# Optimization experiments

Measured on AMD Instinct MI355X. Metric: run time of the kernel, lower is better.

## Reference

```python
import jax, jax.numpy as jnp
import numpy as np

H = 1024      # hidden_size
I = 2048      # intermediate_size
E = 32        # num_routed_experts
B, S = 4, 2048


def setup_inputs() -> dict:
    key = jax.random.key(0)
    ks = jax.random.split(key, 8)
    scale = 0.02
    inp = {
        "hidden_states": jax.random.normal(ks[0], (B, S, H), dtype=jnp.float32),
        # router gate: stored [H, E] so logits = x @ gate_w
        "gate_w": jax.random.normal(ks[1], (H, E), dtype=jnp.float32) * scale,
        # shared SwiGLU (num_shared_experts=1), weights stored [in, out]
        "shared_gate_w": jax.random.normal(ks[2], (H, I), dtype=jnp.float32) * scale,
        "shared_up_w": jax.random.normal(ks[3], (H, I), dtype=jnp.float32) * scale,
        "shared_down_w": jax.random.normal(ks[4], (I, H), dtype=jnp.float32) * scale,
        # routed grouped SwiGLU, weights stored [E, in, out] (matches GroupedLinear)
        "routed_gate_w": jax.random.normal(ks[5], (E, H, I), dtype=jnp.float32) * scale,
        "routed_up_w": jax.random.normal(ks[6], (E, H, I), dtype=jnp.float32) * scale,
        "routed_down_w": jax.random.normal(ks[7], (E, I, H), dtype=jnp.float32) * scale,
    }
    return inp


def _grouped_mm(a, w, group_sizes):
    # a: [T, in], w: [E, in, out], group_sizes: [E] int32 -> [T, out]
    return jax.lax.ragged_dot(a, w, group_sizes)


def _swiglu(x, gw, uw, dw):
    return (jax.nn.silu(x @ gw) * (x @ uw)) @ dw


def reference(hidden_states, gate_w, shared_gate_w, shared_up_w, shared_down_w,
              routed_gate_w, routed_up_w, routed_down_w):
    b, s, h = hidden_states.shape
    x = hidden_states.reshape(-1, h)                      # [T, H]

    # ---- shared expert ----
    shared_out = _swiglu(x, shared_gate_w, shared_up_w, shared_down_w)

    # ---- router: top-1 ----
    logits = x @ gate_w                                   # [T, E]
    topk_ids = jnp.argmax(logits, axis=-1)                # [T]
    topk_val = jnp.max(logits, axis=-1)                   # [T]
    scores = jax.nn.sigmoid(topk_val)[:, None]            # [T, 1]
    xs = x * scores                                       # scale tokens by router score

    # ---- dispatch: sort tokens by expert id ----
    tokens_per_expert = jnp.zeros((E,), jnp.int32).at[topk_ids].add(1)
    order = jnp.argsort(topk_ids)                         # token ids sorted by expert
    sorted_x = xs[order]                                  # [T, H]

    # ---- grouped SwiGLU experts ----
    g = _grouped_mm(sorted_x, routed_gate_w, tokens_per_expert)   # [T, I]
    u = _grouped_mm(sorted_x, routed_up_w, tokens_per_expert)     # [T, I]
    d = _grouped_mm(jax.nn.silu(g) * u, routed_down_w, tokens_per_expert)  # [T, H]

    # ---- combine: unsort back to token order ----
    inv = jnp.argsort(order)
    routed_out = d[inv]

    return (shared_out + routed_out).reshape(b, s, h)
```

## Files before the change

### kernel.cpp

```cpp
#include <hip/hip_runtime.h>
#include <stdint.h>
#include <stddef.h>

#define TOK 8192
#define H 1024
#define IDIM 2048
#define NE 32
#define BM 128
#define BN 64
#define BK 64
#define MAX_TILES 96

typedef __attribute__((ext_vector_type(8))) short short8;
typedef __attribute__((ext_vector_type(4))) float f32x4;
typedef __attribute__((ext_vector_type(4))) float float4v;
typedef __attribute__((ext_vector_type(2))) unsigned int uint2v;
typedef __attribute__((ext_vector_type(4))) unsigned int uint4v;


__device__ __forceinline__ unsigned short f2bf(float x) {
  unsigned u = __builtin_bit_cast(unsigned, x);
  u += 0x7fffu + ((u >> 16) & 1u);
  return (unsigned short)(u >> 16);
}

__device__ __forceinline__ float bf2f(unsigned short h) {
  unsigned u = ((unsigned)h) << 16;
  return __builtin_bit_cast(float, u);
}

__device__ __forceinline__ unsigned cvtpk(float lo, float hi) {
  unsigned r;
  asm("v_cvt_pk_bf16_f32 %0, %1, %2" : "=v"(r) : "v"(lo), "v"(hi));
  return r;
}

__device__ __forceinline__ void gll16(const void* g, void* l) {
  __builtin_amdgcn_global_load_lds(
      (const __attribute__((address_space(1))) unsigned int*)g,
      (__attribute__((address_space(3))) unsigned int*)l, 16, 0, 0);
}

__device__ __forceinline__ f32x4 mfma16(short8 a, short8 b, f32x4 c) {
  return __builtin_amdgcn_mfma_f32_16x16x32_bf16(a, b, c, 0, 0, 0);
}

__device__ __forceinline__ int wswz(int n) {
  return ((n ^ (n >> 2)) & 7) << 4;
}


__global__ __launch_bounds__(256) void router_kernel(
    const float* __restrict__ x, const float* __restrict__ gw,
    unsigned short* __restrict__ xbf, unsigned short* __restrict__ xsbf,
    int* __restrict__ expert_id, int* __restrict__ counts)
{
  __shared__ float xl[8 * H];
  __shared__ float plog[8][8][NE];
  __shared__ float sscore[8];
  const int tid = threadIdx.x;
  const long t0 = (long)blockIdx.x * 8;

  const float4v* src = (const float4v*)(x + t0 * H);
  float4v* dst = (float4v*)xl;
  #pragma unroll
  for (int i = 0; i < 8; ++i) dst[tid + i * 256] = src[tid + i * 256];
  __syncthreads();

  {
    const int e = tid & 31, c = tid >> 5;
    float acc[8] = {0, 0, 0, 0, 0, 0, 0, 0};
    const float* gp = gw + (c * 128) * NE + e;
    for (int h = 0; h < 128; ++h) {
      float g = gp[h * NE];
      const float* xr = xl + (c * 128 + h);
      #pragma unroll
      for (int tk = 0; tk < 8; ++tk) acc[tk] += xr[tk * H] * g;
    }
    #pragma unroll
    for (int tk = 0; tk < 8; ++tk) plog[c][tk][e] = acc[tk];
  }
  __syncthreads();
  {
    const int e = tid & 31, tok = tid >> 5;
    float lg = 0.f;
    #pragma unroll
    for (int c = 0; c < 8; ++c) lg += plog[c][tok][e];
    float m = lg; int be = e;
    #pragma unroll
    for (int mask = 16; mask >= 1; mask >>= 1) {
      float om = __shfl_xor(m, mask);
      int   oe = __shfl_xor(be, mask);
      if (om > m || (om == m && oe < be)) { m = om; be = oe; }
    }
    if (e == 0) {
      sscore[tok] = 1.f / (1.f + __expf(-m));
      expert_id[t0 + tok] = be;
      atomicAdd(&counts[be], 1);
    }
  }
  __syncthreads();
  {
    const float sc = sscore[tid >> 5];
    const int base = (tid >> 5) * H + (tid & 31) * 32;
    #pragma unroll
    for (int i = 0; i < 4; ++i) {
      uint4v vx, vs;
      #pragma unroll
      for (int q = 0; q < 4; ++q) {
        const float a = xl[base + i * 8 + 2 * q];
        const float b = xl[base + i * 8 + 2 * q + 1];
        vx[q] = cvtpk(a, b);
        vs[q] = cvtpk(a * sc, b * sc);
      }
      *(uint4v*)(xbf  + t0 * H + base + i * 8) = vx;
      *(uint4v*)(xsbf + t0 * H + base + i * 8) = vs;
    }
  }
}


__global__ void scan_kernel(const int* __restrict__ counts, int* __restrict__ offsets,
                            int* __restrict__ cursor, int* __restrict__ tile_e,
                            int* __restrict__ tile_p, int* __restrict__ n_tiles)
{
  if (threadIdx.x != 0) return;
  int off = 0, nt = 0;
  for (int e = 0; e < NE; ++e) {
    offsets[e] = off; cursor[e] = off;
    int cc = counts[e];
    for (int k = 0; k < cc; k += BM) { tile_e[nt] = e; tile_p[nt] = off + k; ++nt; }
    off += cc;
  }
  offsets[NE] = off;
  n_tiles[0] = nt;
}


__global__ __launch_bounds__(256) void perm_kernel(
    const int* __restrict__ expert_id, int* __restrict__ cursor, int* __restrict__ perm)
{
  int t = blockIdx.x * 256 + threadIdx.x;
  int e = expert_id[t];
  int pos = atomicAdd(&cursor[e], 1);
  perm[pos] = t;
}


template<bool ROUTED, bool APERM, int KD, int ND, int EPI>
__global__ __launch_bounds__(256, 4) void gemm_kernel(
    const unsigned short* __restrict__ A,
    const float* __restrict__ Wall,
    float* __restrict__ outf,
    unsigned short* __restrict__ outh,
    const int* __restrict__ perm, const int* __restrict__ tile_e,
    const int* __restrict__ tile_p, const int* __restrict__ offsets,
    const int* __restrict__ n_tiles)
{
  __shared__ short Alds[2][BM * BK];
  __shared__ short Wlds[BN * BK];

  const int tid = threadIdx.x;
  const int wave = tid >> 6, lane = tid & 63;

  int row0, row_end;
  const float* W;
  if constexpr (ROUTED) {
    if ((int)blockIdx.x >= *n_tiles) return;
    const int e = tile_e[blockIdx.x];
    row0 = tile_p[blockIdx.x];
    row_end = offsets[e + 1];
    W = Wall + (size_t)e * KD * ND;
  } else {
    row0 = blockIdx.x * BM; row_end = row0 + BM;
    W = Wall;
  }
  const int n0 = blockIdx.y * BN;

  const unsigned short* asrc[4];
  int aoff[4];
  #pragma unroll
  for (int i = 0; i < 4; ++i) {
    const int r = wave * 32 + i * 8 + (lane >> 3);
    int p = row0 + r;
    if (ROUTED && p >= row_end) p = row0;
    int grow = p;
    if constexpr (ROUTED && APERM) grow = perm[p];
    const int cb = ((lane & 7) * 16) ^ ((r & 7) << 4);
    asrc[i] = A + (size_t)grow * KD + (cb >> 1);
    aoff[i] = (wave * 32 + i * 8) * BK;
  }

  const int wq = tid >> 4;
  const int wc = tid & 15;

  f32x4 acc[2][4] = {};
  float4v w4[4];

  auto stageA = [&](int kt) {
    short* base = Alds[kt & 1];
    #pragma unroll
    for (int i = 0; i < 4; ++i) gll16(asrc[i] + kt * BK, base + aoff[i]);
  };
  auto loadW = [&](int kt) {
    const int k0 = kt * BK;
    #pragma unroll
    for (int r = 0; r < 4; ++r)
      w4[r] = *(const float4v*)(W + (size_t)(k0 + wq * 4 + r) * ND + (n0 + wc * 4));
  };
  auto writeW = [&]() {
    #pragma unroll
    for (int j = 0; j < 4; ++j) {
      const int n = wc * 4 + j;
      const int cb = (wq * 8) ^ wswz(n);
      uint2v pw;
      pw.x = cvtpk(w4[0][j], w4[1][j]);
      pw.y = cvtpk(w4[2][j], w4[3][j]);
      *(uint2v*)((char*)Wlds + n * 128 + cb) = pw;
    }
  };
  auto compute = [&](int kt) {
    const char* ab = (const char*)Alds[kt & 1];
    #pragma unroll
    for (int kk = 0; kk < 2; ++kk) {
      short8 af[2];
      #pragma unroll
      for (int m = 0; m < 2; ++m) {
        const int r = wave * 32 + m * 16 + (lane & 15);
        const int cb = (kk * 64 + ((lane >> 4) * 16)) ^ ((r & 7) << 4);
        af[m] = *(const short8*)(ab + r * 128 + cb);
      }
      #pragma unroll
      for (int nf = 0; nf < 4; ++nf) {
        const int n = nf * 16 + (lane & 15);
        const int cb = (kk * 64 + ((lane >> 4) * 16)) ^ wswz(n);
        short8 bw = *(const short8*)((const char*)Wlds + n * 128 + cb);
        #pragma unroll
        for (int m = 0; m < 2; ++m) acc[m][nf] = mfma16(af[m], bw, acc[m][nf]);
      }
    }
  };

  stageA(0);
  loadW(0);
  writeW();
  __syncthreads();

  #pragma unroll 1
  for (int kt = 0; kt < KD / BK - 1; ++kt) {
    stageA(kt + 1);
    loadW(kt + 1);
    compute(kt);
    __syncthreads();
    writeW();
    __syncthreads();
  }
  compute(KD / BK - 1);

  #pragma unroll
  for (int m = 0; m < 2; ++m)
    #pragma unroll
    for (int nf = 0; nf < 4; ++nf) {
      const int col = n0 + nf * 16 + (lane & 15);
      #pragma unroll
      for (int j = 0; j < 4; ++j) {
        const int row = row0 + wave * 32 + m * 16 + ((lane >> 4) * 4) + j;
        if (ROUTED && row >= row_end) continue;
        const float v = acc[m][nf][j];
        if constexpr (EPI == 0) {
          outh[(size_t)row * ND + col] = f2bf(v);
        } else if constexpr (EPI == 1) {
          const float u = bf2f(outh[(size_t)row * ND + col]);
          const float s = v / (1.f + __expf(-v));
          outh[(size_t)row * ND + col] = f2bf(s * u);
        } else if constexpr (EPI == 2) {
          outf[(size_t)row * ND + col] = v;
        } else {
          const int t = perm[row];
          outf[(size_t)t * ND + col] += v;
        }
      }
    }
}


extern "C" void kernel_launch(void* const* d_in, const int* in_sizes, int n_in,
                              void* d_out, int out_size, void* d_ws, size_t ws_size,
                              hipStream_t stream) {
  (void)in_sizes; (void)n_in; (void)out_size; (void)ws_size;
  const float* x      = (const float*)d_in[0];
  const float* gate_w = (const float*)d_in[1];
  const float* sgw    = (const float*)d_in[2];
  const float* suw    = (const float*)d_in[3];
  const float* sdw    = (const float*)d_in[4];
  const float* rgw    = (const float*)d_in[5];
  const float* ruw    = (const float*)d_in[6];
  const float* rdw    = (const float*)d_in[7];
  float* out = (float*)d_out;

  char* ws = (char*)d_ws;
  unsigned short* xbf  = (unsigned short*)(ws + 0);
  unsigned short* xsbf = (unsigned short*)(ws + 16777216);
  unsigned short* act  = (unsigned short*)(ws + 33554432);
  int* perm      = (int*)(ws + 67108864);
  int* expert_id = (int*)(ws + 67141632);
  int* counts    = (int*)(ws + 67174400);
  int* offsets   = (int*)(ws + 67174528);
  int* cursor    = (int*)(ws + 67174784);
  int* tile_e    = (int*)(ws + 67174912);
  int* tile_p    = (int*)(ws + 67175424);
  int* n_tiles   = (int*)(ws + 67175936);

  hipMemsetAsync(counts, 0, NE * sizeof(int), stream);
  router_kernel<<<TOK / 8, 256, 0, stream>>>(x, gate_w, xbf, xsbf, expert_id, counts);
  scan_kernel<<<1, 64, 0, stream>>>(counts, offsets, cursor, tile_e, tile_p, n_tiles);
  perm_kernel<<<TOK / 256, 256, 0, stream>>>(expert_id, cursor, perm);

  gemm_kernel<false, false, H, IDIM, 0><<<dim3(TOK / BM, IDIM / BN), 256, 0, stream>>>(
      xbf, suw, nullptr, act, perm, tile_e, tile_p, offsets, n_tiles);
  gemm_kernel<false, false, H, IDIM, 1><<<dim3(TOK / BM, IDIM / BN), 256, 0, stream>>>(
      xbf, sgw, nullptr, act, perm, tile_e, tile_p, offsets, n_tiles);
  gemm_kernel<false, false, IDIM, H, 2><<<dim3(TOK / BM, H / BN), 256, 0, stream>>>(
      act, sdw, out, nullptr, perm, tile_e, tile_p, offsets, n_tiles);

  gemm_kernel<true, true, H, IDIM, 0><<<dim3(MAX_TILES, IDIM / BN), 256, 0, stream>>>(
      xsbf, ruw, nullptr, act, perm, tile_e, tile_p, offsets, n_tiles);
  gemm_kernel<true, true, H, IDIM, 1><<<dim3(MAX_TILES, IDIM / BN), 256, 0, stream>>>(
      xsbf, rgw, nullptr, act, perm, tile_e, tile_p, offsets, n_tiles);
  gemm_kernel<true, false, IDIM, H, 3><<<dim3(MAX_TILES, H / BN), 256, 0, stream>>>(
      act, rdw, out, nullptr, perm, tile_e, tile_p, offsets, n_tiles);
}
```

Before: 742.6 us.

## Pre-transpose weights to bf16 and use 128x128 tiles with async B loads

Adds a transpose-and-convert kernel that writes every weight matrix (shared and all 32 routed experts) as K-contiguous bf16 into workspace on each call. The GEMM then loads both A and B straight into LDS with global_load_lds, computes a 128x128 tile per block (4x4 MFMA fragments per wave), and applies a grid swizzle for L2 locality. This drops the in-loop fp32 load, convert and LDS write of weights, but adds a full read of all fp32 weights plus a bf16 write each call (about 800MB of traffic even for experts that receive no tokens), and it removes the double-buffered A pipeline.

```diff
diff --git a/kernel.cpp b/kernel.cpp
--- a/kernel.cpp
+++ b/kernel.cpp
@@ -7,14 +7,12 @@
 #define IDIM 2048
 #define NE 32
 #define BM 128
-#define BN 64
 #define BK 64
 #define MAX_TILES 96
 
 typedef __attribute__((ext_vector_type(8))) short short8;
 typedef __attribute__((ext_vector_type(4))) float f32x4;
 typedef __attribute__((ext_vector_type(4))) float float4v;
-typedef __attribute__((ext_vector_type(2))) unsigned int uint2v;
 typedef __attribute__((ext_vector_type(4))) unsigned int uint4v;
 
 
@@ -45,8 +43,43 @@
   return __builtin_amdgcn_mfma_f32_16x16x32_bf16(a, b, c, 0, 0, 0);
 }
 
-__device__ __forceinline__ int wswz(int n) {
-  return ((n ^ (n >> 2)) & 7) << 4;
+
+__global__ __launch_bounds__(256) void tconv_kernel(
+    const float* __restrict__ src0, unsigned short* __restrict__ dst0,
+    int K, int N)
+{
+  __shared__ float t[64][65];
+  const size_t mat = (size_t)K * N;
+  const float* src = src0 + (size_t)blockIdx.z * mat;
+  unsigned short* dst = dst0 + (size_t)blockIdx.z * mat;
+  const int k0 = blockIdx.x * 64, n0 = blockIdx.y * 64;
+  const int tid = threadIdx.x;
+  {
+    const int r = tid >> 4;
+    const int c = (tid & 15) * 4;
+    #pragma unroll
+    for (int i = 0; i < 4; ++i) {
+      float4v v = *(const float4v*)(src + (size_t)(k0 + r + i * 16) * N + (n0 + c));
+      t[r + i * 16][c + 0] = v[0];
+      t[r + i * 16][c + 1] = v[1];
+      t[r + i * 16][c + 2] = v[2];
+      t[r + i * 16][c + 3] = v[3];
+    }
+  }
+  __syncthreads();
+  {
+    const int n = tid >> 2;
+    const int kc = (tid & 3) * 16;
+    uint4v o0, o1;
+    #pragma unroll
+    for (int q = 0; q < 4; ++q) {
+      o0[q] = cvtpk(t[kc + 2 * q][n],     t[kc + 2 * q + 1][n]);
+      o1[q] = cvtpk(t[kc + 8 + 2 * q][n], t[kc + 8 + 2 * q + 1][n]);
+    }
+    unsigned short* dp = dst + (size_t)(n0 + n) * K + (k0 + kc);
+    *(uint4v*)dp = o0;
+    *(uint4v*)(dp + 8) = o1;
+  }
 }
 
 
@@ -148,123 +181,96 @@
 
 
 template<bool ROUTED, bool APERM, int KD, int ND, int EPI>
-__global__ __launch_bounds__(256, 4) void gemm_kernel(
+__global__ __launch_bounds__(256, 4) void bgemm_kernel(
     const unsigned short* __restrict__ A,
-    const float* __restrict__ Wall,
+    const unsigned short* __restrict__ BT,
     float* __restrict__ outf,
     unsigned short* __restrict__ outh,
     const int* __restrict__ perm, const int* __restrict__ tile_e,
     const int* __restrict__ tile_p, const int* __restrict__ offsets,
     const int* __restrict__ n_tiles)
 {
-  __shared__ short Alds[2][BM * BK];
-  __shared__ short Wlds[BN * BK];
+  __shared__ short Al[BM * BK];
+  __shared__ short Bl[128 * BK];
 
   const int tid = threadIdx.x;
   const int wave = tid >> 6, lane = tid & 63;
+  const int wm = wave >> 1, wn = wave & 1;
+
+  const int nx = gridDim.x;
+  const int nwg = nx * gridDim.y;
+  const int flat = blockIdx.y * nx + blockIdx.x;
+  const int swz = (flat & 7) * (nwg >> 3) + (flat >> 3);
+  const int bx = swz % nx, by = swz / nx;
 
   int row0, row_end;
-  const float* W;
+  const unsigned short* Bt;
   if constexpr (ROUTED) {
-    if ((int)blockIdx.x >= *n_tiles) return;
-    const int e = tile_e[blockIdx.x];
-    row0 = tile_p[blockIdx.x];
+    if (bx >= *n_tiles) return;
+    const int e = tile_e[bx];
+    row0 = tile_p[bx];
     row_end = offsets[e + 1];
-    W = Wall + (size_t)e * KD * ND;
+    Bt = BT + (size_t)e * KD * ND;
   } else {
-    row0 = blockIdx.x * BM; row_end = row0 + BM;
-    W = Wall;
-  }
-  const int n0 = blockIdx.y * BN;
-
-  const unsigned short* asrc[4];
-  int aoff[4];
+    row0 = bx * BM; row_end = row0 + BM;
+    Bt = BT;
+  }
+  const int n0 = by * 128;
+
+  const unsigned short *asrc[4], *bsrc[4];
+  int soff[4];
   #pragma unroll
   for (int i = 0; i < 4; ++i) {
     const int r = wave * 32 + i * 8 + (lane >> 3);
     int p = row0 + r;
     if (ROUTED && p >= row_end) p = row0;
-    int grow = p;
-    if constexpr (ROUTED && APERM) grow = perm[p];
+    int arow = p;
+    if constexpr (ROUTED && APERM) arow = perm[p];
     const int cb = ((lane & 7) * 16) ^ ((r & 7) << 4);
-    asrc[i] = A + (size_t)grow * KD + (cb >> 1);
-    aoff[i] = (wave * 32 + i * 8) * BK;
-  }
-
-  const int wq = tid >> 4;
-  const int wc = tid & 15;
-
-  f32x4 acc[2][4] = {};
-  float4v w4[4];
-
-  auto stageA = [&](int kt) {
-    short* base = Alds[kt & 1];
-    #pragma unroll
-    for (int i = 0; i < 4; ++i) gll16(asrc[i] + kt * BK, base + aoff[i]);
-  };
-  auto loadW = [&](int kt) {
-    const int k0 = kt * BK;
-    #pragma unroll
-    for (int r = 0; r < 4; ++r)
-      w4[r] = *(const float4v*)(W + (size_t)(k0 + wq * 4 + r) * ND + (n0 + wc * 4));
-  };
-  auto writeW = [&]() {
-    #pragma unroll
-    for (int j = 0; j < 4; ++j) {
-      const int n = wc * 4 + j;
-      const int cb = (wq * 8) ^ wswz(n);
-      uint2v pw;
-      pw.x = cvtpk(w4[0][j], w4[1][j]);
-      pw.y = cvtpk(w4[2][j], w4[3][j]);
-      *(uint2v*)((char*)Wlds + n * 128 + cb) = pw;
-    }
-  };
-  auto compute = [&](int kt) {
-    const char* ab = (const char*)Alds[kt & 1];
+    asrc[i] = A  + (size_t)arow * KD + (cb >> 1);
+    bsrc[i] = Bt + (size_t)(n0 + r) * KD + (cb >> 1);
+    soff[i] = (wave * 32 + i * 8) * BK;
+  }
+
+  f32x4 acc[4][4] = {};
+
+  #pragma unroll 1
+  for (int kt = 0; kt < KD / BK; ++kt) {
+    __syncthreads();
+    #pragma unroll
+    for (int i = 0; i < 4; ++i) gll16(asrc[i] + kt * BK, Al + soff[i]);
+    #pragma unroll
+    for (int i = 0; i < 4; ++i) gll16(bsrc[i] + kt * BK, Bl + soff[i]);
+    __syncthreads();
+
     #pragma unroll
     for (int kk = 0; kk < 2; ++kk) {
-      short8 af[2];
-      #pragma unroll
-      for (int m = 0; m < 2; ++m) {
-        const int r = wave * 32 + m * 16 + (lane & 15);
+      short8 af[4];
+      #pragma unroll
+      for (int m = 0; m < 4; ++m) {
+        const int r = wm * 64 + m * 16 + (lane & 15);
         const int cb = (kk * 64 + ((lane >> 4) * 16)) ^ ((r & 7) << 4);
-        af[m] = *(const short8*)(ab + r * 128 + cb);
+        af[m] = *(const short8*)((const char*)Al + r * 128 + cb);
       }
       #pragma unroll
       for (int nf = 0; nf < 4; ++nf) {
-        const int n = nf * 16 + (lane & 15);
-        const int cb = (kk * 64 + ((lane >> 4) * 16)) ^ wswz(n);
-        short8 bw = *(const short8*)((const char*)Wlds + n * 128 + cb);
+        const int n = wn * 64 + nf * 16 + (lane & 15);
+        const int cb = (kk * 64 + ((lane >> 4) * 16)) ^ ((n & 7) << 4);
+        short8 bw = *(const short8*)((const char*)Bl + n * 128 + cb);
         #pragma unroll
-        for (int m = 0; m < 2; ++m) acc[m][nf] = mfma16(af[m], bw, acc[m][nf]);
+        for (int m = 0; m < 4; ++m) acc[m][nf] = mfma16(af[m], bw, acc[m][nf]);
       }
     }
-  };
-
-  stageA(0);
-  loadW(0);
-  writeW();
-  __syncthreads();
-
-  #pragma unroll 1
-  for (int kt = 0; kt < KD / BK - 1; ++kt) {
-    stageA(kt + 1);
-    loadW(kt + 1);
-    compute(kt);
-    __syncthreads();
-    writeW();
-    __syncthreads();
-  }
-  compute(KD / BK - 1);
+  }
 
   #pragma unroll
-  for (int m = 0; m < 2; ++m)
+  for (int m = 0; m < 4; ++m)
     #pragma unroll
     for (int nf = 0; nf < 4; ++nf) {
-      const int col = n0 + nf * 16 + (lane & 15);
+      const int col = n0 + wn * 64 + nf * 16 + (lane & 15);
       #pragma unroll
       for (int j = 0; j < 4; ++j) {
-        const int row = row0 + wave * 32 + m * 16 + ((lane >> 4) * 4) + j;
+        const int row = row0 + wm * 64 + m * 16 + ((lane >> 4) * 4) + j;
         if (ROUTED && row >= row_end) continue;
         const float v = acc[m][nf][j];
         if constexpr (EPI == 0) {
@@ -310,23 +316,36 @@
   int* tile_e    = (int*)(ws + 67174912);
   int* tile_p    = (int*)(ws + 67175424);
   int* n_tiles   = (int*)(ws + 67175936);
+  unsigned short* rgwT = (unsigned short*)(ws + 68157440);
+  unsigned short* ruwT = (unsigned short*)(ws + 202375168);
+  unsigned short* rdwT = (unsigned short*)(ws + 336592896);
+  unsigned short* sgwT = (unsigned short*)(ws + 470810624);
+  unsigned short* suwT = (unsigned short*)(ws + 475004928);
+  unsigned short* sdwT = (unsigned short*)(ws + 479199232);
 
   hipMemsetAsync(counts, 0, NE * sizeof(int), stream);
+
   router_kernel<<<TOK / 8, 256, 0, stream>>>(x, gate_w, xbf, xsbf, expert_id, counts);
   scan_kernel<<<1, 64, 0, stream>>>(counts, offsets, cursor, tile_e, tile_p, n_tiles);
   perm_kernel<<<TOK / 256, 256, 0, stream>>>(expert_id, cursor, perm);
 
-  gemm_kernel<false, false, H, IDIM, 0><<<dim3(TOK / BM, IDIM / BN), 256, 0, stream>>>(
-      xbf, suw, nullptr, act, perm, tile_e, tile_p, offsets, n_tiles);
-  gemm_kernel<false, false, H, IDIM, 1><<<dim3(TOK / BM, IDIM / BN), 256, 0, stream>>>(
-      xbf, sgw, nullptr, act, perm, tile_e, tile_p, offsets, n_tiles);
-  gemm_kernel<false, false, IDIM, H, 2><<<dim3(TOK / BM, H / BN), 256, 0, stream>>>(
-      act, sdw, out, nullptr, perm, tile_e, tile_p, offsets, n_tiles);
-
-  gemm_kernel<true, true, H, IDIM, 0><<<dim3(MAX_TILES, IDIM / BN), 256, 0, stream>>>(
-      xsbf, ruw, nullptr, act, perm, tile_e, tile_p, offsets, n_tiles);
-  gemm_kernel<true, true, H, IDIM, 1><<<dim3(MAX_TILES, IDIM / BN), 256, 0, stream>>>(
-      xsbf, rgw, nullptr, act, perm, tile_e, tile_p, offsets, n_tiles);
-  gemm_kernel<true, false, IDIM, H, 3><<<dim3(MAX_TILES, H / BN), 256, 0, stream>>>(
-      act, rdw, out, nullptr, perm, tile_e, tile_p, offsets, n_tiles);
-}
+  tconv_kernel<<<dim3(H / 64, IDIM / 64, 1), 256, 0, stream>>>(suw, suwT, H, IDIM);
+  tconv_kernel<<<dim3(H / 64, IDIM / 64, 1), 256, 0, stream>>>(sgw, sgwT, H, IDIM);
+  tconv_kernel<<<dim3(IDIM / 64, H / 64, 1), 256, 0, stream>>>(sdw, sdwT, IDIM, H);
+  bgemm_kernel<false, false, H, IDIM, 0><<<dim3(TOK / BM, IDIM / 128), 256, 0, stream>>>(
+      xbf, suwT, nullptr, act, perm, tile_e, tile_p, offsets, n_tiles);
+  bgemm_kernel<false, false, H, IDIM, 1><<<dim3(TOK / BM, IDIM / 128), 256, 0, stream>>>(
+      xbf, sgwT, nullptr, act, perm, tile_e, tile_p, offsets, n_tiles);
+  bgemm_kernel<false, false, IDIM, H, 2><<<dim3(TOK / BM, H / 128), 256, 0, stream>>>(
+      act, sdwT, out, nullptr, perm, tile_e, tile_p, offsets, n_tiles);
+
+  tconv_kernel<<<dim3(H / 64, IDIM / 64, NE), 256, 0, stream>>>(ruw, ruwT, H, IDIM);
+  bgemm_kernel<true, true, H, IDIM, 0><<<dim3(MAX_TILES, IDIM / 128), 256, 0, stream>>>(
+      xsbf, ruwT, nullptr, act, perm, tile_e, tile_p, offsets, n_tiles);
+  tconv_kernel<<<dim3(H / 64, IDIM / 64, NE), 256, 0, stream>>>(rgw, rgwT, H, IDIM);
+  bgemm_kernel<true, true, H, IDIM, 1><<<dim3(MAX_TILES, IDIM / 128), 256, 0, stream>>>(
+      xsbf, rgwT, nullptr, act, perm, tile_e, tile_p, offsets, n_tiles);
+  tconv_kernel<<<dim3(IDIM / 64, H / 64, NE), 256, 0, stream>>>(rdw, rdwT, IDIM, H);
+  bgemm_kernel<true, false, IDIM, H, 3><<<dim3(MAX_TILES, H / 128), 256, 0, stream>>>(
+      act, rdwT, out, nullptr, perm, tile_e, tile_p, offsets, n_tiles);
+}
```

New measurement: 755.4 us. No clear change (+1.7%).
